# Performance work log

Measured on AMD Instinct MI355X. Metric: run time of the kernel, lower is better.

Reference implementation:

```python
import jax, jax.numpy as jnp
import numpy as np

D = 512
H = 2048
L = 8192
NSEG = 16
LN_EPS = 1e-6  # flax LayerNorm default


def _ln_tokens(x):
    # flax LayerNorm(reduction_axes=-2, feature_axes=-1, use_bias=False, use_scale=False):
    # mean/var reduced over the token axis (-2), per feature; no learned params.
    mu = jnp.mean(x, axis=-2, keepdims=True)
    var = jnp.var(x, axis=-2, keepdims=True)
    return (x - mu) * jax.lax.rsqrt(var + LN_EPS)


def setup_inputs() -> dict:
    key = jax.random.key(0)
    ks = jax.random.split(key, 8)
    xcat = jax.random.normal(ks[0], (L, D), dtype=jnp.float32)
    xsep = jnp.sort(jax.random.randint(ks[1], (L,), 0, NSEG)).astype(jnp.int64)
    s = 0.02
    Wqkv = jax.random.normal(ks[2], (D, 3 * D), dtype=jnp.float32) * s
    bqkv = jnp.zeros((3 * D,), dtype=jnp.float32)
    W1 = jax.random.normal(ks[3], (D, H), dtype=jnp.float32) * s
    b1 = jnp.zeros((H,), dtype=jnp.float32)
    W2 = jax.random.normal(ks[4], (H, D), dtype=jnp.float32) * s
    b2 = jnp.zeros((D,), dtype=jnp.float32)
    return {"xcat": xcat, "xsep": xsep, "Wqkv": Wqkv, "bqkv": bqkv,
            "W1": W1, "b1": b1, "W2": W2, "b2": b2}


def reference(xcat, xsep, Wqkv, bqkv, W1, b1, W2, b2):
    Ltok = xcat.shape[0]
    qkv = _ln_tokens(xcat) @ Wqkv + bqkv            # [L, 3D]
    q = qkv[:, :D]
    k = qkv[:, D:2 * D]
    # v = qkv[:, 2*D:3*D]  # computed in original but never used
    # unscaled scores; softmax FIRST, then mask, then renormalize (faithful to source)
    atten = jax.nn.softmax(jnp.einsum('id,jd->ij', q, k), axis=-1)  # [L, L]
    idx = jnp.arange(Ltok)
    mask = (xsep[None, :] == xsep[:, None]) & (idx[None, :] <= idx[:, None])
    atten = atten * mask
    atten = atten / (atten.sum(axis=-1, keepdims=True) + 1e-10)
    ctx = atten @ xcat                               # attention applied to raw xcat
    ffn = jax.nn.relu(_ln_tokens(ctx) @ W1 + b1) @ W2 + b2
    return (xcat + ffn, xsep)
```

## Files before the change

### kernel.cpp

```cpp
#include <hip/hip_runtime.h>
#include <math.h>

#define LTOK 8192
#define DDIM 512
#define HDIM 2048
#define NSEG 16
#define DCUT 128
#define ZROWS (NSEG * DCUT)
#define ZCH 64
#define NPART (ZCH * 4)
#define BM 128
#define BN 128
#define BK 64
#define PW 1280
#define PTILES (PW / BN)

typedef float f32x4 __attribute__((ext_vector_type(4)));
typedef short s16x8 __attribute__((ext_vector_type(8)));

static __device__ __forceinline__ short f2bf(float f) {
    union { float f; unsigned u; } v; v.f = f;
    unsigned r = (v.u + 0x7fffu + ((v.u >> 16) & 1u)) >> 16;
    return (short)r;
}
static __device__ __forceinline__ float bf2f(short s) {
    union { unsigned u; float f; } v;
    v.u = ((unsigned)(unsigned short)s) << 16;
    return v.f;
}

template<int GX, int GY>
__device__ __forceinline__ void swz_xslow(int& x, int& y) {
    constexpr int cpx = (GX * GY) >> 3;
    const int orig = blockIdx.y * GX + blockIdx.x;
    const int lg = (orig & 7) * cpx + (orig >> 3);
    x = lg / GY;
    y = lg - x * GY;
}
template<int GX, int GY>
__device__ __forceinline__ void swz_yslow(int& x, int& y) {
    constexpr int cpx = (GX * GY) >> 3;
    const int orig = blockIdx.y * GX + blockIdx.x;
    const int lg = (orig & 7) * cpx + (orig >> 3);
    y = lg / GX;
    x = lg - y * GX;
}

__global__ void ln_stats_partial(const float* __restrict__ X,
                                 float* __restrict__ psum, float* __restrict__ psumsq) {
    int c = threadIdx.x;
    int b = blockIdx.x;
    const float* p = X + (size_t)b * 256 * DDIM + c;
    float s = 0.f, s2 = 0.f;
    for (int r = 0; r < 256; ++r) {
        float v = p[(size_t)r * DDIM];
        s += v; s2 += v * v;
    }
    psum[b * DDIM + c] = s;
    psumsq[b * DDIM + c] = s2;
}

__global__ void ln_stats_final(const float* __restrict__ psum, const float* __restrict__ psumsq,
                               float* __restrict__ mu, float* __restrict__ rstd) {
    int c = threadIdx.x;
    float s = 0.f, s2 = 0.f;
    for (int b = 0; b < 32; ++b) { s += psum[b * DDIM + c]; s2 += psumsq[b * DDIM + c]; }
    float m = s / (float)LTOK;
    float var = s2 / (float)LTOK - m * m;
    mu[c] = m;
    rstd[c] = rsqrtf(var + 1e-6f);
}

__global__ void ln_apply_bf16(const float* __restrict__ X,
                              const float* __restrict__ mu, const float* __restrict__ rstd,
                              short* __restrict__ out) {
    int t = blockIdx.x * 256 + threadIdx.x;
    int base = t * 4;
    int c = base & (DDIM - 1);
    float4 v = *(const float4*)(X + base);
    short4 o;
    o.x = f2bf((v.x - mu[c + 0]) * rstd[c + 0]);
    o.y = f2bf((v.y - mu[c + 1]) * rstd[c + 1]);
    o.z = f2bf((v.z - mu[c + 2]) * rstd[c + 2]);
    o.w = f2bf((v.w - mu[c + 3]) * rstd[c + 3]);
    *(short4*)(out + base) = o;
}

__global__ void transpose_w(const float* __restrict__ W, int ldw, int n0,
                            short* __restrict__ WT, int R) {
    __shared__ short t[32][33];
    int nb = n0 + blockIdx.x * 32;
    int rb = blockIdx.y * 32;
    int tx = threadIdx.x & 31, ty = threadIdx.x >> 5;
    for (int rr = ty; rr < 32; rr += 8)
        t[rr][tx] = f2bf(W[(size_t)(rb + rr) * ldw + nb + tx]);
    __syncthreads();
    for (int rr = ty; rr < 32; rr += 8)
        WT[(size_t)(nb - n0 + rr) * R + rb + tx] = t[tx][rr];
}

__global__ void transpose_bf16(const float* __restrict__ X, short* __restrict__ XT) {
    __shared__ short t[32][33];
    int c0 = blockIdx.x * 32;
    int r0 = blockIdx.y * 32;
    int tx = threadIdx.x & 31, ty = threadIdx.x >> 5;
    for (int rr = ty; rr < 32; rr += 8)
        t[rr][tx] = f2bf(X[(size_t)(r0 + rr) * DDIM + c0 + tx]);
    __syncthreads();
    for (int rr = ty; rr < 32; rr += 8)
        XT[(size_t)(c0 + rr) * LTOK + r0 + tx] = t[tx][rr];
}

__global__ void seg_begin_k(const int* __restrict__ sep, int* __restrict__ begin,
                            float* __restrict__ out2) {
    int i = blockIdx.x * 256 + threadIdx.x;
    if (i < LTOK) {
        if (i == 0 || sep[i] != sep[i - 1]) begin[sep[i]] = i;
        out2[i] = (float)sep[i];
    }
}

__global__ void gather_qz(const short* __restrict__ qk, const int* __restrict__ sep,
                          const int* __restrict__ begin, short* __restrict__ qg) {
    const int gi = blockIdx.x;
    const int s = gi >> 7, d = gi & (DCUT - 1);
    const int r = begin[s] + d;
    if ((unsigned)r < LTOK && sep[r] == s) {
        const short2* src = (const short2*)(qk + (size_t)r * 1024);
        short2* dst = (short2*)(qg + (size_t)gi * DDIM);
        dst[threadIdx.x] = src[threadIdx.x];
    }
}

__device__ __forceinline__ void stage_tile512(const short* __restrict__ src, int lda,
                                              short* lds, int tid) {
    const int wave = tid >> 6;
    const int lane = tid & 63;
    #pragma unroll
    for (int u = 0; u < 2; ++u) {
        const int c = u * 512 + wave * 64 + lane;
        const short* g = src + (size_t)(c >> 3) * lda + (c & 7) * 8;
        short* l = lds + (size_t)(u * 512 + wave * 64) * 8;
        __builtin_amdgcn_global_load_lds(
            (const __attribute__((address_space(1))) unsigned int*)g,
            (__attribute__((address_space(3))) unsigned int*)l,
            16, 0, 0);
    }
}

__device__ __forceinline__ void mma8_step(const short (*As)[BK], const short (*Bs)[BK],
                                          f32x4 acc[4][2], int wr, int wc, int grp, int lrow) {
    #pragma unroll
    for (int kk = 0; kk < 2; ++kk) {
        s16x8 af[4], bfr[2];
        #pragma unroll
        for (int f = 0; f < 4; ++f)
            af[f] = *(const s16x8*)&As[wr * 64 + f * 16 + lrow][grp * 8 + kk * 32];
        #pragma unroll
        for (int f = 0; f < 2; ++f)
            bfr[f] = *(const s16x8*)&Bs[wc * 32 + f * 16 + lrow][grp * 8 + kk * 32];
        #pragma unroll
        for (int fm = 0; fm < 4; ++fm)
            #pragma unroll
            for (int fn = 0; fn < 2; ++fn)
                acc[fm][fn] = __builtin_amdgcn_mfma_f32_16x16x32_bf16(
                    af[fm], bfr[fn], acc[fm][fn], 0, 0, 0);
    }
}

template<int EPI, int GX, int GY>
__global__ __launch_bounds__(512) void mm_bt8(const short* __restrict__ A, int lda,
        const short* __restrict__ BT, int ldb,
        const float* __restrict__ bias, const float* __restrict__ resid,
        float* __restrict__ Cf, short* __restrict__ Cb, int ldc, int K) {
    __shared__ short As[BM][BK];
    __shared__ short Bs[BN][BK];
    const int tid = threadIdx.x;
    const int wave = tid >> 6, lane = tid & 63, grp = lane >> 4, lrow = lane & 15;
    const int wr = wave >> 2, wc = wave & 3;
    int bx, by;
    swz_yslow<GX, GY>(bx, by);
    const int m0 = by * BM, n0 = bx * BN;
    if (EPI == 3) {
        A += (size_t)blockIdx.z * K;
        BT += (size_t)blockIdx.z * K;
    }
    f32x4 acc[4][2];
    #pragma unroll
    for (int a = 0; a < 4; ++a)
        #pragma unroll
        for (int b = 0; b < 2; ++b) acc[a][b] = (f32x4){0.f, 0.f, 0.f, 0.f};
    for (int k0 = 0; k0 < K; k0 += BK) {
        __syncthreads();
        stage_tile512(A + (size_t)m0 * lda + k0, lda, &As[0][0], tid);
        stage_tile512(BT + (size_t)n0 * ldb + k0, ldb, &Bs[0][0], tid);
        asm volatile("s_waitcnt vmcnt(0)" ::: "memory");
        __syncthreads();
        mma8_step(As, Bs, acc, wr, wc, grp, lrow);
    }
    #pragma unroll
    for (int fm = 0; fm < 4; ++fm) {
        #pragma unroll
        for (int i = 0; i < 4; ++i) {
            int row = m0 + wr * 64 + fm * 16 + grp * 4 + i;
            #pragma unroll
            for (int fn = 0; fn < 2; ++fn) {
                int col = n0 + wc * 32 + fn * 16 + lrow;
                float v = acc[fm][fn][i] + (EPI == 3 ? 0.f : bias[col]);
                if (EPI == 1) v = fmaxf(v, 0.f);
                if (EPI == 2) {
                    Cf[(size_t)row * ldc + col] = v + resid[(size_t)row * ldc + col];
                } else if (EPI == 3) {
                    Cb[(size_t)blockIdx.z * ((size_t)LTOK * ldc)
                       + (size_t)row * ldc + col] = f2bf(v);
                } else {
                    Cb[(size_t)row * ldc + col] = f2bf(v);
                }
            }
        }
    }
}

__global__ void ffn2_combine(const short* __restrict__ hp, const float* __restrict__ b2,
                             const float* __restrict__ xcat, float* __restrict__ out) {
    const int t = blockIdx.x * 256 + threadIdx.x;
    const int base = t * 4;
    const int c = base & (DDIM - 1);
    float4 r = *(const float4*)(xcat + base);
    float4 a;
    a.x = r.x + b2[c + 0];
    a.y = r.y + b2[c + 1];
    a.z = r.z + b2[c + 2];
    a.w = r.w + b2[c + 3];
    #pragma unroll
    for (int z = 0; z < 4; ++z) {
        short4 p = *(const short4*)(hp + (size_t)z * LTOK * DDIM + base);
        a.x += bf2f(p.x); a.y += bf2f(p.y); a.z += bf2f(p.z); a.w += bf2f(p.w);
    }
    *(float4*)(out + base) = a;
}

__global__ __launch_bounds__(512) void attn_zg(const short* __restrict__ qg,
        const short* __restrict__ qk, float* __restrict__ Zg) {
    __shared__ short As[BM][BK];
    __shared__ short Bs[BN][BK];
    const int tid = threadIdx.x;
    const int wave = tid >> 6, lane = tid & 63, grp = lane >> 4, lrow = lane & 15;
    const int wr = wave >> 2, wc = wave & 3;
    int bx, by;
    swz_xslow<ZCH, ZROWS / BM>(bx, by);
    const int g0 = by * BM;
    const int j0 = bx * BN;
    f32x4 acc[4][2];
    #pragma unroll
    for (int a = 0; a < 4; ++a)
        #pragma unroll
        for (int b = 0; b < 2; ++b) acc[a][b] = (f32x4){0.f, 0.f, 0.f, 0.f};
    for (int k0 = 0; k0 < DDIM; k0 += BK) {
        __syncthreads();
        stage_tile512(qg + (size_t)g0 * DDIM + k0, DDIM, &As[0][0], tid);
        stage_tile512(qk + (size_t)j0 * 1024 + 512 + k0, 1024, &Bs[0][0], tid);
        asm volatile("s_waitcnt vmcnt(0)" ::: "memory");
        __syncthreads();
        mma8_step(As, Bs, acc, wr, wc, grp, lrow);
    }
    #pragma unroll
    for (int idx = 0; idx < 16; ++idx) {
        float z = __expf(acc[idx >> 2][0][idx & 3]) + __expf(acc[idx >> 2][1][idx & 3]);
        #pragma unroll
        for (int off = 1; off < 16; off <<= 1) z += __shfl_xor(z, off, 16);
        if (lrow == 0) {
            const int gi = g0 + wr * 64 + (idx >> 2) * 16 + grp * 4 + (idx & 3);
            Zg[(size_t)gi * NPART + bx * 4 + wc] = z;
        }
    }
}

__global__ __launch_bounds__(512) void attn_sp(const short* __restrict__ qk,
        const int* __restrict__ sep, const int* __restrict__ begin,
        short* __restrict__ P) {
    __shared__ short As[BM][BK];
    __shared__ short Bs[BN][BK];
    const int tid = threadIdx.x;
    const int wave = tid >> 6, lane = tid & 63, grp = lane >> 4, lrow = lane & 15;
    const int wr = wave >> 2, wc = wave & 3;
    int bx, by;
    swz_yslow<PTILES, 64>(bx, by);
    const int m0 = by * BM;
    const int jb0 = begin[sep[m0]] & ~(BN - 1);
    const int j0 = jb0 + bx * BN;
    if (j0 >= m0 + BM) return;
    f32x4 acc[4][2];
    #pragma unroll
    for (int a = 0; a < 4; ++a)
        #pragma unroll
        for (int b = 0; b < 2; ++b) acc[a][b] = (f32x4){0.f, 0.f, 0.f, 0.f};
    for (int k0 = 0; k0 < DDIM; k0 += BK) {
        __syncthreads();
        stage_tile512(qk + (size_t)m0 * 1024 + k0, 1024, &As[0][0], tid);
        stage_tile512(qk + (size_t)j0 * 1024 + 512 + k0, 1024, &Bs[0][0], tid);
        asm volatile("s_waitcnt vmcnt(0)" ::: "memory");
        __syncthreads();
        mma8_step(As, Bs, acc, wr, wc, grp, lrow);
    }
    #pragma unroll
    for (int fm = 0; fm < 4; ++fm) {
        #pragma unroll
        for (int i = 0; i < 4; ++i) {
            const int row = m0 + wr * 64 + fm * 16 + grp * 4 + i;
            short* pr = P + (size_t)row * PW + (j0 - jb0) + wc * 32;
            #pragma unroll
            for (int fn = 0; fn < 2; ++fn)
                pr[fn * 16 + lrow] = f2bf(__expf(acc[fm][fn][i]));
        }
    }
}

__global__ void mask_inv(short* __restrict__ P,
                         const int* __restrict__ sep, const int* __restrict__ begin,
                         const float* __restrict__ Zg, float* __restrict__ invE) {
    const int wv = threadIdx.x >> 6, lane = threadIdx.x & 63;
    const int r = blockIdx.x * 4 + wv;
    const int m0 = r & ~(BM - 1);
    const int jb0 = begin[sep[m0]] & ~(BN - 1);
    const int kw = m0 + BM - jb0;
    const int sr = sep[r];
    const int jsr = begin[sr];
    short* Pr = P + (size_t)r * PW;
    float e = 0.f;
    for (int c = lane * 2; c < kw; c += 128) {
        short2 v = *(short2*)(Pr + c);
        const int col0 = jb0 + c;
        float p0 = bf2f(v.x), p1 = bf2f(v.y);
        if (col0 < jsr || col0 > r) { p0 = 0.f; v.x = 0; }
        if (col0 + 1 < jsr || col0 + 1 > r) { p1 = 0.f; v.y = 0; }
        e += p0 + p1;
        *(short2*)(Pr + c) = v;
    }
    const int d = r - jsr;
    float z = 0.f;
    if (d < DCUT) {
        const float* zr = Zg + (size_t)(sr * DCUT + d) * NPART;
        #pragma unroll
        for (int c = 0; c < NPART / 64; ++c) z += zr[c * 64 + lane];
    }
    #pragma unroll
    for (int off = 1; off < 64; off <<= 1) {
        e += __shfl_xor(e, off);
        z += __shfl_xor(z, off);
    }
    if (lane == 0) invE[r] = 1.f / (e + 1e-10f * z);
}

__global__ __launch_bounds__(512) void attn_pv(const short* __restrict__ P,
        const short* __restrict__ xbT,
        const int* __restrict__ sep, const int* __restrict__ begin,
        const float* __restrict__ invE, float* __restrict__ ctx) {
    __shared__ short As[BM][BK];
    __shared__ short Bs[BN][BK];
    const int tid = threadIdx.x;
    const int wave = tid >> 6, lane = tid & 63, grp = lane >> 4, lrow = lane & 15;
    const int wr = wave >> 2, wc = wave & 3;
    int bx, by;
    swz_yslow<4, 64>(bx, by);
    const int m0 = by * BM, n0 = bx * BN;
    const int jbase0 = begin[sep[m0]] & ~(BN - 1);
    const int kmax = m0 + BM - jbase0;
    f32x4 acc[4][2];
    #pragma unroll
    for (int a = 0; a < 4; ++a)
        #pragma unroll
        for (int b = 0; b < 2; ++b) acc[a][b] = (f32x4){0.f, 0.f, 0.f, 0.f};
    for (int k0 = 0; k0 < kmax; k0 += BK) {
        __syncthreads();
        stage_tile512(P + (size_t)m0 * PW + k0, PW, &As[0][0], tid);
        stage_tile512(xbT + (size_t)n0 * LTOK + jbase0 + k0, LTOK, &Bs[0][0], tid);
        asm volatile("s_waitcnt vmcnt(0)" ::: "memory");
        __syncthreads();
        mma8_step(As, Bs, acc, wr, wc, grp, lrow);
    }
    #pragma unroll
    for (int fm = 0; fm < 4; ++fm) {
        #pragma unroll
        for (int i = 0; i < 4; ++i) {
            int row = m0 + wr * 64 + fm * 16 + grp * 4 + i;
            float inv = invE[row];
            #pragma unroll
            for (int fn = 0; fn < 2; ++fn) {
                int col = n0 + wc * 32 + fn * 16 + lrow;
                ctx[(size_t)row * DDIM + col] = acc[fm][fn][i] * inv;
            }
        }
    }
}

extern "C" void kernel_launch(void* const* d_in, const int* in_sizes, int n_in,
                              void* d_out, int out_size, void* d_ws, size_t ws_size,
                              hipStream_t stream) {
    const float* xcat = (const float*)d_in[0];
    const int* sep = (const int*)d_in[1];
    const float* Wqkv = (const float*)d_in[2];
    const float* bqkv = (const float*)d_in[3];
    const float* W1 = (const float*)d_in[4];
    const float* b1 = (const float*)d_in[5];
    const float* W2 = (const float*)d_in[6];
    const float* b2 = (const float*)d_in[7];
    float* out = (float*)d_out;

    float* ws = (float*)d_ws;
    float* psum   = ws;
    float* psumsq = psum + 32 * DDIM;
    float* mu1    = psumsq + 32 * DDIM;
    float* rstd1  = mu1 + DDIM;
    float* mu2    = rstd1 + DDIM;
    float* rstd2  = mu2 + DDIM;
    float* invE   = rstd2 + DDIM;
    float* Zg     = invE + LTOK;
    int*   begin  = (int*)(Zg + (size_t)ZROWS * NPART);
    short* qg     = (short*)(begin + 1024);
    short* qk     = qg    + (size_t)ZROWS * DDIM;
    short* xbT    = qk    + (size_t)LTOK * 1024;
    short* lnx    = xbT   + (size_t)DDIM * LTOK;
    short* lnctx  = lnx   + (size_t)LTOK * DDIM;
    short* hb     = lnctx + (size_t)LTOK * DDIM;
    short* Pbuf   = hb;
    short* WqkvT  = hb    + (size_t)LTOK * HDIM;
    short* W1T    = WqkvT + (size_t)1024 * DDIM;
    short* W2T    = W1T   + (size_t)HDIM * DDIM;
    float* ctxF   = (float*)(W2T + (size_t)DDIM * HDIM);
    short* hpart  = qk;

    ln_stats_partial<<<dim3(32), dim3(512), 0, stream>>>(xcat, psum, psumsq);
    ln_stats_final<<<dim3(1), dim3(512), 0, stream>>>(psum, psumsq, mu1, rstd1);
    ln_apply_bf16<<<dim3(LTOK * DDIM / 4 / 256), dim3(256), 0, stream>>>(xcat, mu1, rstd1, lnx);

    transpose_w<<<dim3(32, 16), dim3(256), 0, stream>>>(Wqkv, 3 * DDIM, 0, WqkvT, DDIM);
    transpose_w<<<dim3(64, 16), dim3(256), 0, stream>>>(W1, HDIM, 0, W1T, DDIM);
    transpose_w<<<dim3(16, 64), dim3(256), 0, stream>>>(W2, DDIM, 0, W2T, HDIM);

    mm_bt8<0, 8, 64><<<dim3(8, 64), dim3(512), 0, stream>>>(
        lnx, DDIM, WqkvT, DDIM, bqkv, (const float*)nullptr,
        (float*)nullptr, qk, 1024, DDIM);

    seg_begin_k<<<dim3(32), dim3(256), 0, stream>>>(sep, begin, out + (size_t)LTOK * DDIM);
    transpose_bf16<<<dim3(16, 256), dim3(256), 0, stream>>>(xcat, xbT);

    gather_qz<<<dim3(ZROWS), dim3(256), 0, stream>>>(qk, sep, begin, qg);
    attn_zg<<<dim3(ZCH, ZROWS / BM), dim3(512), 0, stream>>>(qg, qk, Zg);

    attn_sp<<<dim3(PTILES, 64), dim3(512), 0, stream>>>(qk, sep, begin, Pbuf);
    mask_inv<<<dim3(LTOK / 4), dim3(256), 0, stream>>>(Pbuf, sep, begin, Zg, invE);
    attn_pv<<<dim3(4, 64), dim3(512), 0, stream>>>(Pbuf, xbT, sep, begin, invE, ctxF);

    ln_stats_partial<<<dim3(32), dim3(512), 0, stream>>>(ctxF, psum, psumsq);
    ln_stats_final<<<dim3(1), dim3(512), 0, stream>>>(psum, psumsq, mu2, rstd2);
    ln_apply_bf16<<<dim3(LTOK * DDIM / 4 / 256), dim3(256), 0, stream>>>(ctxF, mu2, rstd2, lnctx);

    mm_bt8<1, 16, 64><<<dim3(16, 64), dim3(512), 0, stream>>>(
        lnctx, DDIM, W1T, DDIM, b1, (const float*)nullptr,
        (float*)nullptr, hb, HDIM, DDIM);

    mm_bt8<3, 4, 64><<<dim3(4, 64, 4), dim3(512), 0, stream>>>(
        hb, HDIM, W2T, HDIM, (const float*)nullptr, (const float*)nullptr,
        (float*)nullptr, hpart, DDIM, HDIM / 4);
    ffn2_combine<<<dim3(LTOK * DDIM / 4 / 256), dim3(256), 0, stream>>>(hpart, b2, xcat, out);
}
```

Measured before the change: 227.6 us.

## Merge Z-partition and score-tile kernels into one interleaved launch, halve DCUT

Combines the attn_zg and attn_sp kernels into a single launch whose blocks are interleaved 4:5, so both GEMM workloads share the GPU and fill each other's tail, saving one launch and its drain gap. DCUT drops from 128 to 64, halving the gathered-query rows used for the softmax normalizer partial sums, which halves attn_zg work. Fewer sampled rows could affect the correctness of the normalizer if later code assumes the larger cut.

```diff
diff --git a/kernel.cpp b/kernel.cpp
--- a/kernel.cpp
+++ b/kernel.cpp
@@ -5,7 +5,7 @@
 #define DDIM 512
 #define HDIM 2048
 #define NSEG 16
-#define DCUT 128
+#define DCUT 64
 #define ZROWS (NSEG * DCUT)
 #define ZCH 64
 #define NPART (ZCH * 4)
@@ -14,6 +14,8 @@
 #define BK 64
 #define PW 1280
 #define PTILES (PW / BN)
+#define ZGB (ZCH * (ZROWS / BM))
+#define SPB (PTILES * 64)
 
 typedef float f32x4 __attribute__((ext_vector_type(4)));
 typedef short s16x8 __attribute__((ext_vector_type(8)));
@@ -29,14 +31,6 @@
     return v.f;
 }
 
-template<int GX, int GY>
-__device__ __forceinline__ void swz_xslow(int& x, int& y) {
-    constexpr int cpx = (GX * GY) >> 3;
-    const int orig = blockIdx.y * GX + blockIdx.x;
-    const int lg = (orig & 7) * cpx + (orig >> 3);
-    x = lg / GY;
-    y = lg - x * GY;
-}
 template<int GX, int GY>
 __device__ __forceinline__ void swz_yslow(int& x, int& y) {
     constexpr int cpx = (GX * GY) >> 3;
@@ -123,7 +117,7 @@
 __global__ void gather_qz(const short* __restrict__ qk, const int* __restrict__ sep,
                           const int* __restrict__ begin, short* __restrict__ qg) {
     const int gi = blockIdx.x;
-    const int s = gi >> 7, d = gi & (DCUT - 1);
+    const int s = gi / DCUT, d = gi - s * DCUT;
     const int r = begin[s] + d;
     if ((unsigned)r < LTOK && sep[r] == s) {
         const short2* src = (const short2*)(qk + (size_t)r * 1024);
@@ -240,78 +234,77 @@
     *(float4*)(out + base) = a;
 }
 
-__global__ __launch_bounds__(512) void attn_zg(const short* __restrict__ qg,
-        const short* __restrict__ qk, float* __restrict__ Zg) {
+__global__ __launch_bounds__(512) void attn_zgsp(const short* __restrict__ qg,
+        const short* __restrict__ qk,
+        const int* __restrict__ sep, const int* __restrict__ begin,
+        short* __restrict__ P, float* __restrict__ Zg) {
     __shared__ short As[BM][BK];
     __shared__ short Bs[BN][BK];
     const int tid = threadIdx.x;
     const int wave = tid >> 6, lane = tid & 63, grp = lane >> 4, lrow = lane & 15;
     const int wr = wave >> 2, wc = wave & 3;
-    int bx, by;
-    swz_xslow<ZCH, ZROWS / BM>(bx, by);
-    const int g0 = by * BM;
-    const int j0 = bx * BN;
+    const int bid = blockIdx.x;
+    const int grpi = bid / 9, rem = bid - grpi * 9;
     f32x4 acc[4][2];
     #pragma unroll
     for (int a = 0; a < 4; ++a)
         #pragma unroll
         for (int b = 0; b < 2; ++b) acc[a][b] = (f32x4){0.f, 0.f, 0.f, 0.f};
-    for (int k0 = 0; k0 < DDIM; k0 += BK) {
-        __syncthreads();
-        stage_tile512(qg + (size_t)g0 * DDIM + k0, DDIM, &As[0][0], tid);
-        stage_tile512(qk + (size_t)j0 * 1024 + 512 + k0, 1024, &Bs[0][0], tid);
-        asm volatile("s_waitcnt vmcnt(0)" ::: "memory");
-        __syncthreads();
-        mma8_step(As, Bs, acc, wr, wc, grp, lrow);
-    }
-    #pragma unroll
-    for (int idx = 0; idx < 16; ++idx) {
-        float z = __expf(acc[idx >> 2][0][idx & 3]) + __expf(acc[idx >> 2][1][idx & 3]);
-        #pragma unroll
-        for (int off = 1; off < 16; off <<= 1) z += __shfl_xor(z, off, 16);
-        if (lrow == 0) {
-            const int gi = g0 + wr * 64 + (idx >> 2) * 16 + grp * 4 + (idx & 3);
-            Zg[(size_t)gi * NPART + bx * 4 + wc] = z;
-        }
-    }
-}
-
-__global__ __launch_bounds__(512) void attn_sp(const short* __restrict__ qk,
-        const int* __restrict__ sep, const int* __restrict__ begin,
-        short* __restrict__ P) {
-    __shared__ short As[BM][BK];
-    __shared__ short Bs[BN][BK];
-    const int tid = threadIdx.x;
-    const int wave = tid >> 6, lane = tid & 63, grp = lane >> 4, lrow = lane & 15;
-    const int wr = wave >> 2, wc = wave & 3;
-    int bx, by;
-    swz_yslow<PTILES, 64>(bx, by);
-    const int m0 = by * BM;
-    const int jb0 = begin[sep[m0]] & ~(BN - 1);
-    const int j0 = jb0 + bx * BN;
-    if (j0 >= m0 + BM) return;
-    f32x4 acc[4][2];
-    #pragma unroll
-    for (int a = 0; a < 4; ++a)
-        #pragma unroll
-        for (int b = 0; b < 2; ++b) acc[a][b] = (f32x4){0.f, 0.f, 0.f, 0.f};
-    for (int k0 = 0; k0 < DDIM; k0 += BK) {
-        __syncthreads();
-        stage_tile512(qk + (size_t)m0 * 1024 + k0, 1024, &As[0][0], tid);
-        stage_tile512(qk + (size_t)j0 * 1024 + 512 + k0, 1024, &Bs[0][0], tid);
-        asm volatile("s_waitcnt vmcnt(0)" ::: "memory");
-        __syncthreads();
-        mma8_step(As, Bs, acc, wr, wc, grp, lrow);
-    }
-    #pragma unroll
-    for (int fm = 0; fm < 4; ++fm) {
-        #pragma unroll
-        for (int i = 0; i < 4; ++i) {
-            const int row = m0 + wr * 64 + fm * 16 + grp * 4 + i;
-            short* pr = P + (size_t)row * PW + (j0 - jb0) + wc * 32;
+
+    if (rem < 4) {
+        const int orig = grpi * 4 + rem;
+        constexpr int cpx = ZGB >> 3;
+        const int lg = (orig & 7) * cpx + (orig >> 3);
+        const int bx = lg / (ZROWS / BM);
+        const int by = lg - bx * (ZROWS / BM);
+        const int g0 = by * BM;
+        const int j0 = bx * BN;
+        for (int k0 = 0; k0 < DDIM; k0 += BK) {
+            __syncthreads();
+            stage_tile512(qg + (size_t)g0 * DDIM + k0, DDIM, &As[0][0], tid);
+            stage_tile512(qk + (size_t)j0 * 1024 + 512 + k0, 1024, &Bs[0][0], tid);
+            asm volatile("s_waitcnt vmcnt(0)" ::: "memory");
+            __syncthreads();
+            mma8_step(As, Bs, acc, wr, wc, grp, lrow);
+        }
+        #pragma unroll
+        for (int idx = 0; idx < 16; ++idx) {
+            float z = __expf(acc[idx >> 2][0][idx & 3]) + __expf(acc[idx >> 2][1][idx & 3]);
             #pragma unroll
-            for (int fn = 0; fn < 2; ++fn)
-                pr[fn * 16 + lrow] = f2bf(__expf(acc[fm][fn][i]));
+            for (int off = 1; off < 16; off <<= 1) z += __shfl_xor(z, off, 16);
+            if (lrow == 0) {
+                const int gi = g0 + wr * 64 + (idx >> 2) * 16 + grp * 4 + (idx & 3);
+                Zg[(size_t)gi * NPART + bx * 4 + wc] = z;
+            }
+        }
+    } else {
+        const int orig = grpi * 5 + (rem - 4);
+        constexpr int cpx = SPB >> 3;
+        const int lg = (orig & 7) * cpx + (orig >> 3);
+        const int by = lg / PTILES;
+        const int bx = lg - by * PTILES;
+        const int m0 = by * BM;
+        const int jb0 = begin[sep[m0]] & ~(BN - 1);
+        const int j0 = jb0 + bx * BN;
+        if (j0 >= m0 + BM) return;
+        for (int k0 = 0; k0 < DDIM; k0 += BK) {
+            __syncthreads();
+            stage_tile512(qk + (size_t)m0 * 1024 + k0, 1024, &As[0][0], tid);
+            stage_tile512(qk + (size_t)j0 * 1024 + 512 + k0, 1024, &Bs[0][0], tid);
+            asm volatile("s_waitcnt vmcnt(0)" ::: "memory");
+            __syncthreads();
+            mma8_step(As, Bs, acc, wr, wc, grp, lrow);
+        }
+        #pragma unroll
+        for (int fm = 0; fm < 4; ++fm) {
+            #pragma unroll
+            for (int i = 0; i < 4; ++i) {
+                const int row = m0 + wr * 64 + fm * 16 + grp * 4 + i;
+                short* pr = P + (size_t)row * PW + (j0 - jb0) + wc * 32;
+                #pragma unroll
+                for (int fn = 0; fn < 2; ++fn)
+                    pr[fn * 16 + lrow] = f2bf(__expf(acc[fm][fn][i]));
+            }
         }
     }
 }
@@ -446,9 +439,8 @@
     transpose_bf16<<<dim3(16, 256), dim3(256), 0, stream>>>(xcat, xbT);
 
     gather_qz<<<dim3(ZROWS), dim3(256), 0, stream>>>(qk, sep, begin, qg);
-    attn_zg<<<dim3(ZCH, ZROWS / BM), dim3(512), 0, stream>>>(qg, qk, Zg);
-
-    attn_sp<<<dim3(PTILES, 64), dim3(512), 0, stream>>>(qk, sep, begin, Pbuf);
+    attn_zgsp<<<dim3(ZGB + SPB), dim3(512), 0, stream>>>(qg, qk, sep, begin, Pbuf, Zg);
+
     mask_inv<<<dim3(LTOK / 4), dim3(256), 0, stream>>>(Pbuf, sep, begin, Zg, invE);
     attn_pv<<<dim3(4, 64), dim3(512), 0, stream>>>(Pbuf, xbT, sep, begin, invE, ctxF);
 
```

Result: faster. 209.9 us (-7.8%).
